# Kernel tuning notes

Hardware: AMD Instinct MI355X
Metric: run time of the kernel (lower is better)

## Reference

```python
import jax, jax.numpy as jnp
import numpy as np

VOCAB = 65  # 26 + 26 + 10 + 3
EMBED = 6
MAX_CTX = 8192
B, T = 4, 8192


def setup_inputs() -> dict:
    key = jax.random.key(0)
    ks = jax.random.split(key, 8)
    x = jax.random.randint(ks[0], (B, T), 0, VOCAB)
    embed_w = jax.random.normal(ks[1], (VOCAB, EMBED), dtype=jnp.float32)
    # nn.Parameter(torch.tril(torch.rand(...)))
    position_mask = jnp.tril(jax.random.uniform(ks[2], (MAX_CTX, MAX_CTX), dtype=jnp.float32))
    reset_threshold = jax.random.normal(ks[3], (1,), dtype=jnp.float32)
    temperature = jnp.sqrt(jnp.asarray(0.01, dtype=jnp.float32))
    class_transition = jax.random.normal(ks[4], (EMBED, EMBED), dtype=jnp.float32)
    reset_transition = jax.random.normal(ks[5], (EMBED, EMBED), dtype=jnp.float32)
    output = jax.random.normal(ks[6], (EMBED, VOCAB), dtype=jnp.float32)
    return {
        "x": x,
        "embed_w": embed_w,
        "position_mask": position_mask,
        "reset_threshold": reset_threshold,
        "temperature": temperature,
        "class_transition": class_transition,
        "reset_transition": reset_transition,
        "output": output,
    }


def reference(x, embed_w, position_mask, reset_threshold, temperature,
              class_transition, reset_transition, output):
    emb = embed_w[x]                               # [B,T,E]
    class_prob = jax.nn.softmax(emb, axis=-1)      # [B,T,E]
    t = x.shape[1]
    # causal pairwise similarity, weighted and reduced
    sim = jnp.einsum('bte,bse->bts', class_prob, class_prob)   # [B,T,T]
    weights = jnp.tril(position_mask[:t, :t])                  # [T,T]
    score = jnp.sum(sim * weights, axis=-1)                    # [B,T]
    score_scaled = (score - reset_threshold ** 2) / temperature ** 2
    reset = jax.nn.sigmoid(score_scaled)[..., None]            # [B,T,1]
    transition_class = class_prob @ class_transition           # [B,T,E]
    reset_class = class_prob @ reset_transition                # [B,T,E]
    next_class = reset * reset_class + (1.0 - reset) * transition_class
    return next_class @ output                                 # [B,T,V]
```

## Files before the change

kernel.cpp:

```cpp
#include <hip/hip_runtime.h>
#include <cmath>

typedef float f32x4 __attribute__((ext_vector_type(4)));

#define TT 8192
#define NV 65

__device__ __forceinline__ float dot4acc(f32x4 a, f32x4 b, float acc) {
  acc = fmaf(a[0], b[0], acc);
  acc = fmaf(a[1], b[1], acc);
  acc = fmaf(a[2], b[2], acc);
  acc = fmaf(a[3], b[3], acc);
  return acc;
}

__global__ __launch_bounds__(128) void cp_kernel(const int* __restrict__ x,
                                                 const float* __restrict__ ew,
                                                 float* __restrict__ cpt) {
  int n = blockIdx.x * 128 + threadIdx.x;
  int b = n >> 13, t = n & 8191;
  int xv = x[n];
  float v[6];
#pragma unroll
  for (int e = 0; e < 6; ++e) v[e] = ew[xv * 6 + e];
  float m = v[0];
#pragma unroll
  for (int e = 1; e < 6; ++e) m = fmaxf(m, v[e]);
  float s = 0.f;
#pragma unroll
  for (int e = 0; e < 6; ++e) { v[e] = expf(v[e] - m); s += v[e]; }
  float inv = 1.f / s;
#pragma unroll
  for (int e = 0; e < 6; ++e) cpt[(b * 6 + e) * TT + t] = v[e] * inv;
}

__global__ __launch_bounds__(256, 2) void sticky_fused(
    const float* __restrict__ W, const float* __restrict__ cpt,
    const float* __restrict__ rtp, const float* __restrict__ tp,
    const float* __restrict__ CT, const float* __restrict__ RT,
    const float* __restrict__ OM, float* __restrict__ out) {
  __shared__ __align__(16) float cp_lds[24][256];
  __shared__ float ws_lds[4][4][24];
  const int j = blockIdx.x;
  const int tid = threadIdx.x;
  const int w = tid >> 6, lane = tid & 63;
  const int kl = lane * 4;
  const int l0 = 8 * j + 2 * w;
  const int h0 = 8184 - 8 * j + 2 * w;
  const int klow_end = l0 + 2;
  const int k_need = 8192 - 8 * j;
  const int nch = (k_need + 255) >> 8;

  const float* wl = W + (size_t)l0 * TT;
  const float* wh = W + (size_t)h0 * TT;

  float acc[4][24];
#pragma unroll
  for (int r = 0; r < 4; ++r)
#pragma unroll
    for (int e = 0; e < 24; ++e) acc[r][e] = 0.f;

#pragma unroll 1
  for (int ch = 0; ch < nch; ++ch) {
    const int kc = ch << 8;
    __syncthreads();
#pragma unroll
    for (int i = 0; i < 6; ++i) {
      int f = tid + 256 * i;
      int e = f >> 6, c4 = (f & 63) * 4;
      *reinterpret_cast<f32x4*>(&cp_lds[e][c4]) =
          *reinterpret_cast<const f32x4*>(&cpt[e * TT + kc + c4]);
    }
    __syncthreads();
    f32x4 wh0 = __builtin_nontemporal_load(
        reinterpret_cast<const f32x4*>(wh + kc + kl));
    f32x4 wh1 = __builtin_nontemporal_load(
        reinterpret_cast<const f32x4*>(wh + TT + kc + kl));
    if (kc < klow_end) {
      f32x4 wl0 = __builtin_nontemporal_load(
          reinterpret_cast<const f32x4*>(wl + kc + kl));
      f32x4 wl1 = __builtin_nontemporal_load(
          reinterpret_cast<const f32x4*>(wl + TT + kc + kl));
#pragma unroll
      for (int e = 0; e < 24; ++e) {
        f32x4 c = *reinterpret_cast<const f32x4*>(&cp_lds[e][kl]);
        acc[0][e] = dot4acc(wl0, c, acc[0][e]);
        acc[1][e] = dot4acc(wl1, c, acc[1][e]);
        acc[2][e] = dot4acc(wh0, c, acc[2][e]);
        acc[3][e] = dot4acc(wh1, c, acc[3][e]);
      }
    } else {
#pragma unroll
      for (int e = 0; e < 24; ++e) {
        f32x4 c = *reinterpret_cast<const f32x4*>(&cp_lds[e][kl]);
        acc[2][e] = dot4acc(wh0, c, acc[2][e]);
        acc[3][e] = dot4acc(wh1, c, acc[3][e]);
      }
    }
  }

#pragma unroll
  for (int r = 0; r < 4; ++r)
#pragma unroll
    for (int e = 0; e < 24; ++e) {
      float v = acc[r][e];
      v += __shfl_xor(v, 1);
      v += __shfl_xor(v, 2);
      v += __shfl_xor(v, 4);
      v += __shfl_xor(v, 8);
      v += __shfl_xor(v, 16);
      v += __shfl_xor(v, 32);
      acc[r][e] = v;
    }
  if (lane == 0) {
#pragma unroll
    for (int r = 0; r < 4; ++r)
#pragma unroll
      for (int e = 0; e < 24; ++e) ws_lds[w][r][e] = acc[r][e];
  }
  __syncthreads();

  const int rb = lane & 15;
  const int r = rb >> 2, b = rb & 3, vi = lane >> 4;
  const int t = (r < 2) ? (l0 + r) : (h0 + (r - 2));
  float cp6[6], ws6[6];
#pragma unroll
  for (int e = 0; e < 6; ++e) {
    cp6[e] = cpt[(b * 6 + e) * TT + t];
    ws6[e] = ws_lds[w][r][b * 6 + e];
  }
  float score = 0.f;
#pragma unroll
  for (int e = 0; e < 6; ++e) score = fmaf(cp6[e], ws6[e], score);
  float rt = rtp[0];
  float temp = tp[0];
  float z = (score - rt * rt) / (temp * temp);
  float reset = 1.f / (1.f + expf(-z));
  float nc[6];
#pragma unroll
  for (int c = 0; c < 6; ++c) {
    float tc = 0.f, rc = 0.f;
#pragma unroll
    for (int e = 0; e < 6; ++e) {
      tc = fmaf(cp6[e], CT[e * 6 + c], tc);
      rc = fmaf(cp6[e], RT[e * 6 + c], rc);
    }
    nc[c] = reset * rc + (1.f - reset) * tc;
  }
  size_t obase = ((size_t)b * TT + t) * NV;
  for (int v = vi; v < NV; v += 4) {
    float o = 0.f;
#pragma unroll
    for (int c = 0; c < 6; ++c) o = fmaf(nc[c], OM[c * NV + v], o);
    out[obase + v] = o;
  }
}

extern "C" void kernel_launch(void* const* d_in, const int* in_sizes, int n_in,
                              void* d_out, int out_size, void* d_ws, size_t ws_size,
                              hipStream_t stream) {
  const int* x = (const int*)d_in[0];
  const float* ew = (const float*)d_in[1];
  const float* W = (const float*)d_in[2];
  const float* rtp = (const float*)d_in[3];
  const float* tp = (const float*)d_in[4];
  const float* CT = (const float*)d_in[5];
  const float* RT = (const float*)d_in[6];
  const float* OM = (const float*)d_in[7];
  float* out = (float*)d_out;
  float* cpt = (float*)d_ws;

  hipLaunchKernelGGL(cp_kernel, dim3(256), dim3(128), 0, stream, x, ew, cpt);
  hipLaunchKernelGGL(sticky_fused, dim3(512), dim3(256), 0, stream,
                     W, cpt, rtp, tp, CT, RT, OM, out);
}
```

Measured before the change: 76.00 us.

## Double-buffer class-prob LDS tiles and prefetch next mask chunk into registers

Turns the chunk loop into a software pipeline. While the current chunk is being computed, the next chunk's position-mask rows and class-prob tile are loaded into registers, then stored into the second LDS buffer. This drops one barrier per iteration and hides global load latency behind the FMA work. In exchange it uses more registers (extra f32x4 prefetch registers) and twice the LDS, which could lower occupancy under launch_bounds(256,2).

After: 76.21 us. About the same (+0.3%).

```diff
diff --git a/kernel.cpp b/kernel.cpp
--- a/kernel.cpp
+++ b/kernel.cpp
@@ -39,7 +39,7 @@
     const float* __restrict__ rtp, const float* __restrict__ tp,
     const float* __restrict__ CT, const float* __restrict__ RT,
     const float* __restrict__ OM, float* __restrict__ out) {
-  __shared__ __align__(16) float cp_lds[24][256];
+  __shared__ __align__(16) float cp_lds[2][24][256];
   __shared__ float ws_lds[4][4][24];
   const int j = blockIdx.x;
   const int tid = threadIdx.x;
@@ -60,43 +60,88 @@
 #pragma unroll
     for (int e = 0; e < 24; ++e) acc[r][e] = 0.f;
 
-#pragma unroll 1
-  for (int ch = 0; ch < nch; ++ch) {
-    const int kc = ch << 8;
-    __syncthreads();
+  f32x4 whc0 = __builtin_nontemporal_load(reinterpret_cast<const f32x4*>(wh + kl));
+  f32x4 whc1 = __builtin_nontemporal_load(reinterpret_cast<const f32x4*>(wh + TT + kl));
+  f32x4 wlc0 = __builtin_nontemporal_load(reinterpret_cast<const f32x4*>(wl + kl));
+  f32x4 wlc1 = __builtin_nontemporal_load(reinterpret_cast<const f32x4*>(wl + TT + kl));
+  {
+    f32x4 s0[6];
 #pragma unroll
     for (int i = 0; i < 6; ++i) {
       int f = tid + 256 * i;
       int e = f >> 6, c4 = (f & 63) * 4;
-      *reinterpret_cast<f32x4*>(&cp_lds[e][c4]) =
-          *reinterpret_cast<const f32x4*>(&cpt[e * TT + kc + c4]);
-    }
+      s0[i] = *reinterpret_cast<const f32x4*>(&cpt[e * TT + c4]);
+    }
+#pragma unroll
+    for (int i = 0; i < 6; ++i) {
+      int f = tid + 256 * i;
+      int e = f >> 6, c4 = (f & 63) * 4;
+      *reinterpret_cast<f32x4*>(&cp_lds[0][e][c4]) = s0[i];
+    }
+  }
+  __syncthreads();
+
+#pragma unroll 1
+  for (int ch = 0; ch < nch; ++ch) {
+    const int cur = ch & 1;
+    const int kc = ch << 8;
+    const bool hn = (ch + 1 < nch);
+    const int kn = hn ? kc + 256 : kc;
+    const bool lowc = kc < klow_end;
+    const bool lown = kn < klow_end;
+
+    f32x4 whn0 = __builtin_nontemporal_load(
+        reinterpret_cast<const f32x4*>(wh + kn + kl));
+    f32x4 whn1 = __builtin_nontemporal_load(
+        reinterpret_cast<const f32x4*>(wh + TT + kn + kl));
+    f32x4 wln0 = whn0, wln1 = whn1;
+    if (lown) {
+      wln0 = __builtin_nontemporal_load(
+          reinterpret_cast<const f32x4*>(wl + kn + kl));
+      wln1 = __builtin_nontemporal_load(
+          reinterpret_cast<const f32x4*>(wl + TT + kn + kl));
+    }
+    f32x4 sreg[6];
+    if (hn) {
+#pragma unroll
+      for (int i = 0; i < 6; ++i) {
+        int f = tid + 256 * i;
+        int e = f >> 6, c4 = (f & 63) * 4;
+        sreg[i] = *reinterpret_cast<const f32x4*>(&cpt[e * TT + kn + c4]);
+      }
+    }
+
+    if (lowc) {
+#pragma unroll
+      for (int e = 0; e < 24; ++e) {
+        f32x4 c = *reinterpret_cast<const f32x4*>(&cp_lds[cur][e][kl]);
+        acc[0][e] = dot4acc(wlc0, c, acc[0][e]);
+        acc[1][e] = dot4acc(wlc1, c, acc[1][e]);
+        acc[2][e] = dot4acc(whc0, c, acc[2][e]);
+        acc[3][e] = dot4acc(whc1, c, acc[3][e]);
+      }
+    } else {
+#pragma unroll
+      for (int e = 0; e < 24; ++e) {
+        f32x4 c = *reinterpret_cast<const f32x4*>(&cp_lds[cur][e][kl]);
+        acc[2][e] = dot4acc(whc0, c, acc[2][e]);
+        acc[3][e] = dot4acc(whc1, c, acc[3][e]);
+      }
+    }
+
+    if (hn) {
+#pragma unroll
+      for (int i = 0; i < 6; ++i) {
+        int f = tid + 256 * i;
+        int e = f >> 6, c4 = (f & 63) * 4;
+        *reinterpret_cast<f32x4*>(&cp_lds[cur ^ 1][e][c4]) = sreg[i];
+      }
+    }
+    whc0 = whn0;
+    whc1 = whn1;
+    wlc0 = wln0;
+    wlc1 = wln1;
     __syncthreads();
-    f32x4 wh0 = __builtin_nontemporal_load(
-        reinterpret_cast<const f32x4*>(wh + kc + kl));
-    f32x4 wh1 = __builtin_nontemporal_load(
-        reinterpret_cast<const f32x4*>(wh + TT + kc + kl));
-    if (kc < klow_end) {
-      f32x4 wl0 = __builtin_nontemporal_load(
-          reinterpret_cast<const f32x4*>(wl + kc + kl));
-      f32x4 wl1 = __builtin_nontemporal_load(
-          reinterpret_cast<const f32x4*>(wl + TT + kc + kl));
-#pragma unroll
-      for (int e = 0; e < 24; ++e) {
-        f32x4 c = *reinterpret_cast<const f32x4*>(&cp_lds[e][kl]);
-        acc[0][e] = dot4acc(wl0, c, acc[0][e]);
-        acc[1][e] = dot4acc(wl1, c, acc[1][e]);
-        acc[2][e] = dot4acc(wh0, c, acc[2][e]);
-        acc[3][e] = dot4acc(wh1, c, acc[3][e]);
-      }
-    } else {
-#pragma unroll
-      for (int e = 0; e < 24; ++e) {
-        f32x4 c = *reinterpret_cast<const f32x4*>(&cp_lds[e][kl]);
-        acc[2][e] = dot4acc(wh0, c, acc[2][e]);
-        acc[3][e] = dot4acc(wh1, c, acc[3][e]);
-      }
-    }
   }
 
 #pragma unroll
```
